# Optimization experiments

Hardware: AMD Instinct MI355X
Metric: run time of the kernel (lower is better)

The kernel has to match this reference:

```python
import jax, jax.numpy as jnp
import numpy as np


def setup_inputs() -> dict:
    key = jax.random.key(0)
    k1, k2 = jax.random.split(key)
    ns, nd, n_classes = 16384, 2048, 1000
    x = jax.random.normal(k1, (ns, nd), dtype=jnp.float32)
    # prototype means for all seen classes (seen_c == n_classes)
    means = jax.random.normal(k2, (n_classes, nd), dtype=jnp.float32)
    return {"x": x, "means": means, "n_classes": n_classes}


def reference(x, means, n_classes):
    # Original: per-sample dist = -means @ x[s]; argmin(dist) == argmax(means @ x[s]).
    # Batched: one GEMM [ns, nd] x [nd, seen_c] -> scores [ns, seen_c].
    ns = x.shape[0]
    xf = x.reshape(ns, -1)
    scores = jnp.einsum('nd,cd->nc', xf, means)  # [ns, seen_c]
    classpred = jnp.argmax(scores, axis=1)       # argmin of -scores
    out = jax.nn.one_hot(classpred, n_classes, dtype=jnp.float32)  # [ns, n_classes]
    return out
```

## Files before the change

### kernel.cpp

```cpp
#include <hip/hip_runtime.h>
#include <math.h>

#define NS 16384
#define ND 2048
#define NC 1000
#define NCPAD 1024

typedef _Float16 f16x8 __attribute__((ext_vector_type(8)));
typedef _Float16 f16x4 __attribute__((ext_vector_type(4)));
typedef __fp16   h16x2 __attribute__((ext_vector_type(2)));
typedef float f32x4  __attribute__((ext_vector_type(4)));

#define DELTA 2.5f

#define WS_NEW 104857600ull
#define WS_MID 37748736ull

__device__ __forceinline__ void gl_lds16_h(const _Float16* g, _Float16* l) {
    __builtin_amdgcn_global_load_lds(
        (const __attribute__((address_space(1))) unsigned int*)g,
        (__attribute__((address_space(3))) unsigned int*)l, 16, 0, 0);
}
__device__ __forceinline__ void gl_lds16_f(const float* g, float* l) {
    __builtin_amdgcn_global_load_lds(
        (const __attribute__((address_space(1))) unsigned int*)g,
        (__attribute__((address_space(3))) unsigned int*)l, 16, 0, 0);
}

__device__ __forceinline__ f16x8 cvt8(const f32x4 a0, const f32x4 a1) {
    const h16x2 h01 = __builtin_amdgcn_cvt_pkrtz(a0[0], a0[1]);
    const h16x2 h23 = __builtin_amdgcn_cvt_pkrtz(a0[2], a0[3]);
    const h16x2 h45 = __builtin_amdgcn_cvt_pkrtz(a1[0], a1[1]);
    const h16x2 h67 = __builtin_amdgcn_cvt_pkrtz(a1[2], a1[3]);
    f16x8 h;
    h[0]=(_Float16)h01[0]; h[1]=(_Float16)h01[1]; h[2]=(_Float16)h23[0]; h[3]=(_Float16)h23[1];
    h[4]=(_Float16)h45[0]; h[5]=(_Float16)h45[1]; h[6]=(_Float16)h67[0]; h[7]=(_Float16)h67[1];
    return h;
}

__global__ __launch_bounds__(256)
void cvt_all_kernel(const float* __restrict__ x, const float* __restrict__ means,
                    _Float16* __restrict__ xh, _Float16* __restrict__ mhi)
{
    const size_t i = (size_t)blockIdx.x * 256 + threadIdx.x;
    const size_t NM4 = (size_t)NCPAD * ND / 4;
    if (i < NM4) {
        const int row = (int)(i >> 9);
        float4 v = make_float4(0.f, 0.f, 0.f, 0.f);
        if (row < NC) v = ((const float4*)means)[i];
        f16x4 h;
        h[0]=(_Float16)v.x; h[1]=(_Float16)v.y; h[2]=(_Float16)v.z; h[3]=(_Float16)v.w;
        ((f16x4*)mhi)[i] = h;
    } else {
        const size_t j = i - NM4;
        const float4 v = ((const float4*)x)[j];
        f16x4 h;
        h[0]=(_Float16)v.x; h[1]=(_Float16)v.y; h[2]=(_Float16)v.z; h[3]=(_Float16)v.w;
        ((f16x4*)xh)[j] = h;
    }
}

__global__ __launch_bounds__(256, 3)
void gemm_f16_kernel(const _Float16* __restrict__ xh,
                     const _Float16* __restrict__ mhi,
                     _Float16* __restrict__ sc)
{
    __shared__ __align__(16) _Float16 sAh[128 * 32];
    __shared__ __align__(16) _Float16 sBh[128 * 32];

    const int tid  = threadIdx.x;
    const int lane = tid & 63;
    const int w    = tid >> 6;
    const int wm   = w & 1;
    const int wn   = w >> 1;
    const int quad = lane >> 4, l16 = lane & 15;
    const size_t gm0 = (size_t)blockIdx.y * 128;
    const size_t gn0 = (size_t)blockIdx.x * 128;

    f32x4 acc[4][4] = {};

    for (int kt = 0; kt < ND / 32; ++kt) {
        const int k0 = kt * 32;
#pragma unroll
        for (int r = 0; r < 2; ++r) {
            const int slot = r * 256 + tid;
            const int row  = slot >> 2;
            const int ch   = (slot & 3) ^ ((row >> 1) & 3);
            gl_lds16_h(xh  + ((gm0 + row) << 11) + k0 + ch * 8,
                       &sAh[(size_t)(r * 256 + w * 64) * 8]);
            gl_lds16_h(mhi + ((gn0 + row) << 11) + k0 + ch * 8,
                       &sBh[(size_t)(r * 256 + w * 64) * 8]);
        }
        __syncthreads();

        f16x8 ah[4], bh[4];
#pragma unroll
        for (int i = 0; i < 4; ++i) {
            const int ar = wm * 64 + i * 16 + l16;
            const int pc = quad ^ ((ar >> 1) & 3);
            ah[i] = *(const f16x8*)&sAh[ar * 32 + pc * 8];
        }
#pragma unroll
        for (int j = 0; j < 4; ++j) {
            const int br = wn * 64 + j * 16 + l16;
            const int pc = quad ^ ((br >> 1) & 3);
            bh[j] = *(const f16x8*)&sBh[br * 32 + pc * 8];
        }
#pragma unroll
        for (int i = 0; i < 4; ++i)
#pragma unroll
            for (int j = 0; j < 4; ++j)
                acc[i][j] = __builtin_amdgcn_mfma_f32_16x16x32_f16(ah[i], bh[j], acc[i][j], 0, 0, 0);
        __syncthreads();
    }

#pragma unroll
    for (int i = 0; i < 4; ++i) {
        const size_t row0 = gm0 + wm * 64 + i * 16 + quad * 4;
#pragma unroll
        for (int j = 0; j < 4; ++j) {
            const size_t col = gn0 + wn * 64 + j * 16 + l16;
#pragma unroll
            for (int r = 0; r < 4; ++r)
                sc[(row0 + r) * NCPAD + col] = (_Float16)acc[i][j][r];
        }
    }
}

__global__ __launch_bounds__(512, 4)
void gemm_f32a_kernel(const float* __restrict__ x,
                      const _Float16* __restrict__ mhi,
                      _Float16* __restrict__ sc)
{
    __shared__ float    sA [128 * 32];
    __shared__ _Float16 sBh[256 * 32];

    const int tid  = threadIdx.x;
    const int lane = tid & 63;
    const int w    = tid >> 6;
    const int wm   = w & 1;
    const int wn   = w >> 1;
    const int quad = lane >> 4, l16 = lane & 15;
    const size_t gm0 = (size_t)blockIdx.y * 128;
    const size_t gn0 = (size_t)blockIdx.x * 256;

    f32x4 acc[4][4] = {};

    for (int kt = 0; kt < ND / 32; ++kt) {
        const int k0 = kt * 32;
#pragma unroll
        for (int r = 0; r < 2; ++r) {
            const int slot = r * 512 + tid;
            const int arow = slot >> 3;
            const int ac   = (slot & 7) ^ (arow & 7);
            gl_lds16_f(x + ((gm0 + arow) << 11) + k0 + ac * 4,
                       &sA[(r * 512 + w * 64) * 4]);
            const int brow = slot >> 2;
            const int bc   = (slot & 3) ^ ((brow >> 1) & 3);
            gl_lds16_h(mhi + ((gn0 + brow) << 11) + k0 + bc * 8,
                       &sBh[(r * 512 + w * 64) * 8]);
        }
        __syncthreads();

        f16x8 ah[4], bh[4];
#pragma unroll
        for (int i = 0; i < 4; ++i) {
            const int ar = wm * 64 + i * 16 + l16;
            const int c1 = (2 * quad)     ^ (ar & 7);
            const int c2 = (2 * quad + 1) ^ (ar & 7);
            const f32x4 a0 = *(const f32x4*)&sA[ar * 32 + c1 * 4];
            const f32x4 a1 = *(const f32x4*)&sA[ar * 32 + c2 * 4];
            ah[i] = cvt8(a0, a1);
        }
#pragma unroll
        for (int j = 0; j < 4; ++j) {
            const int br = wn * 64 + j * 16 + l16;
            const int pc = quad ^ ((br >> 1) & 3);
            bh[j] = *(const f16x8*)&sBh[br * 32 + pc * 8];
        }
#pragma unroll
        for (int i = 0; i < 4; ++i)
#pragma unroll
            for (int j = 0; j < 4; ++j)
                acc[i][j] = __builtin_amdgcn_mfma_f32_16x16x32_f16(ah[i], bh[j], acc[i][j], 0, 0, 0);
        __syncthreads();
    }

#pragma unroll
    for (int i = 0; i < 4; ++i) {
        const size_t row0 = gm0 + wm * 64 + i * 16 + quad * 4;
#pragma unroll
        for (int j = 0; j < 4; ++j) {
            const size_t col = gn0 + wn * 64 + j * 16 + l16;
#pragma unroll
            for (int r = 0; r < 4; ++r)
                sc[(row0 + r) * NCPAD + col] = (_Float16)acc[i][j][r];
        }
    }
}

__global__ __launch_bounds__(256)
void cvt_m_kernel(const float* __restrict__ src, _Float16* __restrict__ hi)
{
    const int i = blockIdx.x * 256 + threadIdx.x;
    const int row = (i * 4) >> 11;
    float4 v = make_float4(0.f, 0.f, 0.f, 0.f);
    if (row < NC) v = ((const float4*)src)[i];
    f16x4 h;
    h[0] = (_Float16)v.x; h[1] = (_Float16)v.y;
    h[2] = (_Float16)v.z; h[3] = (_Float16)v.w;
    ((f16x4*)hi)[i] = h;
}

__global__ __launch_bounds__(256, 4)
void refine_kernel(const _Float16* __restrict__ sc,
                   const float* __restrict__ x,
                   const float* __restrict__ means,
                   float* __restrict__ out)
{
    const int lane = threadIdx.x & 63;
    const int row  = blockIdx.x * 4 + (threadIdx.x >> 6);

    const f16x8* srow = (const f16x8*)(sc + (size_t)row * NCPAD + lane * 16);
    const f16x8 s0 = srow[0], s1 = srow[1];
    float v[16];
#pragma unroll
    for (int e = 0; e < 8; ++e) { v[e] = (float)s0[e]; v[8 + e] = (float)s1[e]; }

    float mx = -INFINITY;
#pragma unroll
    for (int e = 0; e < 16; ++e) {
        const int c = lane * 16 + e;
        if (c < NC && v[e] > mx) mx = v[e];
    }
#pragma unroll
    for (int off = 1; off < 64; off <<= 1) {
        const float o = __shfl_xor(mx, off);
        if (o > mx) mx = o;
    }
    const float T = mx - DELTA;

    unsigned cm = 0;
#pragma unroll
    for (int e = 0; e < 16; ++e) {
        const int c = lane * 16 + e;
        if (c < NC && v[e] >= T) cm |= (1u << e);
    }

    const unsigned long long bl = __ballot(cm != 0u);
    const int first  = (int)__builtin_ctzll(bl);
    const unsigned cmf = (unsigned)__shfl((int)cm, first);

    int bc;
    if (__builtin_popcountll(bl) == 1 && __builtin_popcount(cmf) == 1) {
        bc = first * 16 + __builtin_ctz(cmf);
    } else {
        const float* xrow = x + ((size_t)row << 11);
        f32x4 xr[8];
#pragma unroll
        for (int it = 0; it < 8; ++it)
            xr[it] = *(const f32x4*)(xrow + it * 256 + lane * 4);

        float bv = -INFINITY;
        bc = 0x7fffffff;
        unsigned long long pend = bl;
        while (pend) {
            const int src = (int)__builtin_ctzll(pend);
            pend &= pend - 1;
            unsigned cms = (unsigned)__shfl((int)cm, src);
            while (cms) {
                const int c = src * 16 + __builtin_ctz(cms);
                cms &= cms - 1;

                const float* mrow = means + ((size_t)c << 11);
                float part = 0.f;
#pragma unroll
                for (int it = 0; it < 8; ++it) {
                    const f32x4 mv = *(const f32x4*)(mrow + it * 256 + lane * 4);
                    part = fmaf(xr[it][0], mv[0], part);
                    part = fmaf(xr[it][1], mv[1], part);
                    part = fmaf(xr[it][2], mv[2], part);
                    part = fmaf(xr[it][3], mv[3], part);
                }
                float s = part;
#pragma unroll
                for (int off = 1; off < 64; off <<= 1) s += __shfl_xor(s, off);

                if (s > bv || (s == bv && c < bc)) { bv = s; bc = c; }
            }
        }
    }

    float4* orow = (float4*)(out + (size_t)row * NC);
#pragma unroll
    for (int i = 0; i < 4; ++i) {
        const int idx = lane + i * 64;
        if (idx < NC / 4) {
            const int cb = idx * 4;
            float4 ov;
            ov.x = (cb     == bc) ? 1.f : 0.f;
            ov.y = (cb + 1 == bc) ? 1.f : 0.f;
            ov.z = (cb + 2 == bc) ? 1.f : 0.f;
            ov.w = (cb + 3 == bc) ? 1.f : 0.f;
            orow[idx] = ov;
        }
    }
}

#define MS 64
#define CS 256
#define KT 32
#define NCHUNK 4

__global__ __launch_bounds__(256, 1)
void nnc_fp32_kernel(const float* __restrict__ x,
                     const float* __restrict__ means,
                     float* __restrict__ out)
{
    __shared__ float xs[MS * KT];
    __shared__ float msh[CS * KT];
    __shared__ float rbest[MS * 33];
    __shared__ int   ridx[MS * 33];
    __shared__ int   widx[MS];

    const int tid = threadIdx.x;
    const int tx  = tid & 31;
    const int ty  = tid >> 5;
    const int s0  = blockIdx.x * MS;
    const int m0  = ty * 8;
    const int cL  = tx * 8;

    float best[8];
    int   bidx[8];
#pragma unroll
    for (int i = 0; i < 8; ++i) { best[i] = -INFINITY; bidx[i] = 0; }

    const int kslot = tid & 7;
    const int rrow  = tid >> 3;

    for (int chunk = 0; chunk < NCHUNK; ++chunk) {
        const int c0 = chunk * CS;
        float acc[8][8];
#pragma unroll
        for (int i = 0; i < 8; ++i)
#pragma unroll
            for (int j = 0; j < 8; ++j) acc[i][j] = 0.0f;

        for (int k0 = 0; k0 < ND; k0 += KT) {
#pragma unroll
            for (int r = 0; r < 2; ++r) {
                const int m = rrow + r * 32;
                const float4 v = *(const float4*)(x + (size_t)(s0 + m) * ND + k0 + kslot * 4);
                *(float4*)(xs + m * KT + kslot * 4) = v;
            }
#pragma unroll
            for (int r = 0; r < 8; ++r) {
                const int c  = rrow + r * 32;
                const int cg = c0 + c;
                float4 v = make_float4(0.f, 0.f, 0.f, 0.f);
                if (cg < NC) v = *(const float4*)(means + (size_t)cg * ND + k0 + kslot * 4);
                const int pslot = (kslot + (c >> 3)) & 7;
                *(float4*)(msh + c * KT + pslot * 4) = v;
            }
            __syncthreads();
#pragma unroll
            for (int k4 = 0; k4 < KT / 4; ++k4) {
                float4 a[8], b[8];
                const int boff = ((k4 + tx) & 7) * 4;
#pragma unroll
                for (int i = 0; i < 8; ++i) a[i] = *(const float4*)(xs + (m0 + i) * KT + k4 * 4);
#pragma unroll
                for (int j = 0; j < 8; ++j) b[j] = *(const float4*)(msh + (cL + j) * KT + boff);
#pragma unroll
                for (int i = 0; i < 8; ++i)
#pragma unroll
                    for (int j = 0; j < 8; ++j) {
                        acc[i][j] = fmaf(a[i].x, b[j].x, acc[i][j]);
                        acc[i][j] = fmaf(a[i].y, b[j].y, acc[i][j]);
                        acc[i][j] = fmaf(a[i].z, b[j].z, acc[i][j]);
                        acc[i][j] = fmaf(a[i].w, b[j].w, acc[i][j]);
                    }
            }
            __syncthreads();
        }
#pragma unroll
        for (int i = 0; i < 8; ++i)
#pragma unroll
            for (int j = 0; j < 8; ++j) {
                const int c = c0 + cL + j;
                const float v = acc[i][j];
                if (c < NC && (v > best[i] || (v == best[i] && c < bidx[i]))) {
                    best[i] = v; bidx[i] = c;
                }
            }
    }
#pragma unroll
    for (int i = 0; i < 8; ++i) {
        rbest[(m0 + i) * 33 + tx] = best[i];
        ridx[(m0 + i) * 33 + tx]  = bidx[i];
    }
    __syncthreads();
    if (tid < MS) {
        float bv = rbest[tid * 33];
        int   bc = ridx[tid * 33];
        for (int t = 1; t < 32; ++t) {
            const float v = rbest[tid * 33 + t];
            const int   c = ridx[tid * 33 + t];
            if (v > bv || (v == bv && c < bc)) { bv = v; bc = c; }
        }
        widx[tid] = bc;
    }
    __syncthreads();
    if (tid < 250) {
        const int cbase = tid * 4;
        for (int m = 0; m < MS; ++m) {
            const int w = widx[m];
            float4 v;
            v.x = (cbase == w) ? 1.f : 0.f;
            v.y = (cbase + 1 == w) ? 1.f : 0.f;
            v.z = (cbase + 2 == w) ? 1.f : 0.f;
            v.w = (cbase + 3 == w) ? 1.f : 0.f;
            *(float4*)(out + (size_t)(s0 + m) * NC + cbase) = v;
        }
    }
}

extern "C" void kernel_launch(void* const* d_in, const int* in_sizes, int n_in,
                              void* d_out, int out_size, void* d_ws, size_t ws_size,
                              hipStream_t stream) {
    const float* x     = (const float*)d_in[0];
    const float* means = (const float*)d_in[1];
    float* out         = (float*)d_out;

    if (ws_size >= WS_NEW) {
        char* ws = (char*)d_ws;
        _Float16* mhi = (_Float16*)ws;
        _Float16* xh  = (_Float16*)(ws + (4ull  << 20));
        _Float16* sc  = (_Float16*)(ws + (68ull << 20));

        cvt_all_kernel<<<dim3((NCPAD * ND / 4 + NS * ND / 4) / 256), dim3(256), 0, stream>>>(x, means, xh, mhi);
        gemm_f16_kernel<<<dim3(NCPAD / 128, NS / 128), dim3(256), 0, stream>>>(xh, mhi, sc);
        refine_kernel<<<dim3(NS / 4), dim3(256), 0, stream>>>(sc, x, means, out);
    } else if (ws_size >= WS_MID) {
        char* ws = (char*)d_ws;
        _Float16* mhi = (_Float16*)ws;
        _Float16* sc  = (_Float16*)(ws + 4194304ull);

        cvt_m_kernel<<<dim3(NCPAD * ND / 4 / 256), dim3(256), 0, stream>>>(means, mhi);
        gemm_f32a_kernel<<<dim3(NCPAD / 256, NS / 128), dim3(512), 0, stream>>>(x, mhi, sc);
        refine_kernel<<<dim3(NS / 4), dim3(256), 0, stream>>>(sc, x, means, out);
    } else {
        nnc_fp32_kernel<<<dim3(NS / MS), dim3(256), 0, stream>>>(x, means, out);
    }
}
```

Measured before the change: 329.7 us.

## Replace fp16 GEMM with 256x256 tile, multi-stage LDS pipelined kernel

Replaces the 128x128 single-buffered fp16 GEMM with a 512-thread 256x256 tile kernel. It double-buffers LDS over K in 64-wide tiles split into two 32-wide halves, issuing async global-to-LDS loads for future stages between MFMA phases using explicit waitcnt and barriers. It also adds a block-index swizzle for L2 locality and s_setprio around the MFMA bursts. The aim is to hide global load latency and raise reuse per loaded byte, at the cost of large LDS use, one block per CU, and fragile hand-written synchronisation.

```diff
diff --git a/kernel.cpp b/kernel.cpp
--- a/kernel.cpp
+++ b/kernel.cpp
@@ -60,69 +60,105 @@
     }
 }
 
-__global__ __launch_bounds__(256, 3)
-void gemm_f16_kernel(const _Float16* __restrict__ xh,
-                     const _Float16* __restrict__ mhi,
-                     _Float16* __restrict__ sc)
-{
-    __shared__ __align__(16) _Float16 sAh[128 * 32];
-    __shared__ __align__(16) _Float16 sBh[128 * 32];
+__device__ __forceinline__ void stage_unit(const _Float16* __restrict__ src,
+                                           size_t g0, _Float16* dstbase,
+                                           int ktile, int kkh, int tid)
+{
+    const int srcT = ktile < 31 ? ktile : 31;
+#pragma unroll
+    for (int q = 0; q < 2; ++q) {
+        const int slot = q * 512 + tid;
+        const int row  = slot >> 2;
+        const int g    = (slot & 3) ^ ((row >> 1) & 3);
+        gl_lds16_h(src + ((g0 + (size_t)row) << 11) + srcT * 64 + kkh * 32 + g * 8,
+                   dstbase + (size_t)(q * 512 + ((tid >> 6) << 6)) * 8);
+    }
+}
+
+__global__ __launch_bounds__(512, 1)
+void gemm256_kernel(const _Float16* __restrict__ xh,
+                    const _Float16* __restrict__ mhi,
+                    _Float16* __restrict__ sc)
+{
+    __shared__ _Float16 sA[2][2][256 * 32];
+    __shared__ _Float16 sB[2][2][256 * 32];
 
     const int tid  = threadIdx.x;
     const int lane = tid & 63;
     const int w    = tid >> 6;
-    const int wm   = w & 1;
-    const int wn   = w >> 1;
+    const int wm   = w >> 2;
+    const int wn   = w & 3;
     const int quad = lane >> 4, l16 = lane & 15;
-    const size_t gm0 = (size_t)blockIdx.y * 128;
-    const size_t gn0 = (size_t)blockIdx.x * 128;
-
-    f32x4 acc[4][4] = {};
-
-    for (int kt = 0; kt < ND / 32; ++kt) {
-        const int k0 = kt * 32;
-#pragma unroll
-        for (int r = 0; r < 2; ++r) {
-            const int slot = r * 256 + tid;
-            const int row  = slot >> 2;
-            const int ch   = (slot & 3) ^ ((row >> 1) & 3);
-            gl_lds16_h(xh  + ((gm0 + row) << 11) + k0 + ch * 8,
-                       &sAh[(size_t)(r * 256 + w * 64) * 8]);
-            gl_lds16_h(mhi + ((gn0 + row) << 11) + k0 + ch * 8,
-                       &sBh[(size_t)(r * 256 + w * 64) * 8]);
-        }
-        __syncthreads();
-
-        f16x8 ah[4], bh[4];
-#pragma unroll
-        for (int i = 0; i < 4; ++i) {
-            const int ar = wm * 64 + i * 16 + l16;
-            const int pc = quad ^ ((ar >> 1) & 3);
-            ah[i] = *(const f16x8*)&sAh[ar * 32 + pc * 8];
-        }
-#pragma unroll
-        for (int j = 0; j < 4; ++j) {
-            const int br = wn * 64 + j * 16 + l16;
-            const int pc = quad ^ ((br >> 1) & 3);
-            bh[j] = *(const f16x8*)&sBh[br * 32 + pc * 8];
-        }
-#pragma unroll
-        for (int i = 0; i < 4; ++i)
-#pragma unroll
-            for (int j = 0; j < 4; ++j)
-                acc[i][j] = __builtin_amdgcn_mfma_f32_16x16x32_f16(ah[i], bh[j], acc[i][j], 0, 0, 0);
-        __syncthreads();
-    }
-
-#pragma unroll
-    for (int i = 0; i < 4; ++i) {
-        const size_t row0 = gm0 + wm * 64 + i * 16 + quad * 4;
+
+    const int orig = blockIdx.x + (blockIdx.y << 2);
+    const int nid  = ((orig & 7) << 5) + (orig >> 3);
+    const size_t gm0 = (size_t)(nid >> 2) * 256;
+    const size_t gn0 = (size_t)(nid & 3) * 256;
+
+    f32x4 acc[8][4] = {};
+
+    stage_unit(xh,  gm0, &sA[0][0][0], 0, 0, tid);
+    stage_unit(mhi, gn0, &sB[0][0][0], 0, 0, tid);
+    stage_unit(xh,  gm0, &sA[0][1][0], 0, 1, tid);
+    stage_unit(mhi, gn0, &sB[0][1][0], 0, 1, tid);
+    stage_unit(xh,  gm0, &sA[1][0][0], 1, 0, tid);
+    stage_unit(mhi, gn0, &sB[1][0][0], 1, 0, tid);
+    asm volatile("s_waitcnt vmcnt(8)" ::: "memory");
+    __builtin_amdgcn_s_barrier();
+
+    f16x8 b[4];
+    for (int kt = 0; kt < 32; ++kt) {
+        const int par = kt & 1;
+#pragma unroll
+        for (int p = 0; p < 4; ++p) {
+            const int mh = p & 1, kk = p >> 1;
+
+            f16x8 a[4];
+#pragma unroll
+            for (int i = 0; i < 4; ++i) {
+                const int ar = wm * 128 + mh * 64 + i * 16 + l16;
+                const int pc = quad ^ ((ar >> 1) & 3);
+                a[i] = *(const f16x8*)&sA[par][kk][ar * 32 + pc * 8];
+            }
+            if (mh == 0) {
+#pragma unroll
+                for (int j = 0; j < 4; ++j) {
+                    const int br = wn * 64 + j * 16 + l16;
+                    const int pc = quad ^ ((br >> 1) & 3);
+                    b[j] = *(const f16x8*)&sB[par][kk][br * 32 + pc * 8];
+                }
+            }
+
+            if (p == 0)      stage_unit(xh,  gm0, &sA[(kt + 1) & 1][1][0], kt + 1, 1, tid);
+            else if (p == 1) stage_unit(mhi, gn0, &sB[(kt + 1) & 1][1][0], kt + 1, 1, tid);
+            else if (p == 2) stage_unit(xh,  gm0, &sA[par][0][0],          kt + 2, 0, tid);
+            else             stage_unit(mhi, gn0, &sB[par][0][0],          kt + 2, 0, tid);
+
+            if (p & 1) asm volatile("s_waitcnt vmcnt(8)" ::: "memory");
+            __builtin_amdgcn_s_barrier();
+            asm volatile("s_waitcnt lgkmcnt(0)" ::: "memory");
+            __builtin_amdgcn_sched_barrier(0);
+            __builtin_amdgcn_s_setprio(1);
+#pragma unroll
+            for (int i = 0; i < 4; ++i)
+#pragma unroll
+                for (int j = 0; j < 4; ++j)
+                    acc[mh * 4 + i][j] =
+                        __builtin_amdgcn_mfma_f32_16x16x32_f16(a[i], b[j], acc[mh * 4 + i][j], 0, 0, 0);
+            __builtin_amdgcn_s_setprio(0);
+            __builtin_amdgcn_s_barrier();
+        }
+    }
+
+#pragma unroll
+    for (int m = 0; m < 8; ++m) {
+        const size_t row0 = gm0 + wm * 128 + m * 16 + quad * 4;
 #pragma unroll
         for (int j = 0; j < 4; ++j) {
             const size_t col = gn0 + wn * 64 + j * 16 + l16;
 #pragma unroll
             for (int r = 0; r < 4; ++r)
-                sc[(row0 + r) * NCPAD + col] = (_Float16)acc[i][j][r];
+                sc[(row0 + r) * NCPAD + col] = (_Float16)acc[m][j][r];
         }
     }
 }
@@ -439,7 +475,7 @@
         _Float16* sc  = (_Float16*)(ws + (68ull << 20));
 
         cvt_all_kernel<<<dim3((NCPAD * ND / 4 + NS * ND / 4) / 256), dim3(256), 0, stream>>>(x, means, xh, mhi);
-        gemm_f16_kernel<<<dim3(NCPAD / 128, NS / 128), dim3(256), 0, stream>>>(xh, mhi, sc);
+        gemm256_kernel<<<dim3(NCPAD / 256, NS / 256), dim3(512), 0, stream>>>(xh, mhi, sc);
         refine_kernel<<<dim3(NS / 4), dim3(256), 0, stream>>>(sc, x, means, out);
     } else if (ws_size >= WS_MID) {
         char* ws = (char*)d_ws;
```

New measurement: 307.5 us. -6.7%, faster.
